# Kernel optimization log

Hardware: AMD Instinct MI355X
Metric: run time of the kernel (lower is better)

## Reference

```python
import jax, jax.numpy as jnp
import numpy as np

EPS = 1e-9

def setup_inputs() -> dict:
    key = jax.random.key(0)
    k1, k2 = jax.random.split(key)
    B = 1048576
    p1 = jax.random.uniform(k1, (B, 10), dtype=jnp.float32)
    p2 = jax.random.uniform(k2, (B, 10), dtype=jnp.float32)
    return {"p1": p1, "p2": p2}

def _sum_bin_matrix(dtype):
    # M[ij, k] = 1 if i + j == k, for flattened 10x10 outer product -> 19 bins
    sum_idx = (jnp.arange(10)[:, None] + jnp.arange(10)[None, :]).reshape(-1)  # [100]
    return (sum_idx[:, None] == jnp.arange(19)[None, :]).astype(dtype)  # [100,19]

def reference(p1, p2):
    B = p1.shape[0]
    # outer product of digit probabilities: T[b,i,j] = p1[b,i] * p2[b,j]
    T = (p1[:, :, None] * p2[:, None, :]).reshape(B, 100)  # [B,100]
    M = _sum_bin_matrix(p1.dtype)  # [100,19]
    probs = T @ M  # [B,19]: per-diagonal sums, P(sum=k)
    probs = probs / (probs.sum(axis=1, keepdims=True) + EPS)
    return probs
```

## Files before the change

kernel.cpp:

```cpp
#include <hip/hip_runtime.h>
#include <stddef.h>


#define EPS 1e-9f

constexpr int THREADS = 256;
constexpr int ROWS    = 256;

__global__ __launch_bounds__(THREADS)
void dpl_add_kernel(const float* __restrict__ p1,
                    const float* __restrict__ p2,
                    float* __restrict__ out,
                    int B) {
    __shared__ __align__(16) float sa[ROWS * 10];
    __shared__ __align__(16) float sb[ROWS * 10];
    __shared__ __align__(16) float so[ROWS * 19];

    const int tid  = threadIdx.x;
    const int row0 = blockIdx.x * ROWS;
    const bool full = (row0 + ROWS) <= B;

    if (full) {
        const float4* g1 = reinterpret_cast<const float4*>(p1 + (size_t)row0 * 10);
        const float4* g2 = reinterpret_cast<const float4*>(p2 + (size_t)row0 * 10);
        float4* s1 = reinterpret_cast<float4*>(sa);
        float4* s2 = reinterpret_cast<float4*>(sb);
        for (int i = tid; i < ROWS * 10 / 4; i += THREADS) {
            s1[i] = g1[i];
            s2[i] = g2[i];
        }
    } else {
        int n = B - row0; if (n < 0) n = 0;
        for (int i = tid; i < n * 10; i += THREADS) {
            sa[i] = p1[(size_t)row0 * 10 + i];
            sb[i] = p2[(size_t)row0 * 10 + i];
        }
    }
    __syncthreads();

    const int b = row0 + tid;
    float s[19];
    #pragma unroll
    for (int k = 0; k < 19; ++k) s[k] = 0.0f;

    if (b < B) {
        float a[10], c[10];
        #pragma unroll
        for (int i = 0; i < 10; ++i) {
            a[i] = sa[tid * 10 + i];
            c[i] = sb[tid * 10 + i];
        }
        #pragma unroll
        for (int i = 0; i < 10; ++i) {
            #pragma unroll
            for (int j = 0; j < 10; ++j) {
                s[i + j] = fmaf(a[i], c[j], s[i + j]);
            }
        }
        float tot = 0.0f;
        #pragma unroll
        for (int k = 0; k < 19; ++k) tot += s[k];
        const float den = tot + EPS;
        #pragma unroll
        for (int k = 0; k < 19; ++k) s[k] = s[k] / den;
    }

    #pragma unroll
    for (int k = 0; k < 19; ++k) so[tid * 19 + k] = s[k];
    __syncthreads();

    if (full) {
        float4* o4 = reinterpret_cast<float4*>(out + (size_t)row0 * 19);
        const float4* s4 = reinterpret_cast<const float4*>(so);
        for (int i = tid; i < ROWS * 19 / 4; i += THREADS) {
            o4[i] = s4[i];
        }
    } else {
        int n = B - row0; if (n < 0) n = 0;
        for (int i = tid; i < n * 19; i += THREADS) {
            out[(size_t)row0 * 19 + i] = so[i];
        }
    }
}

extern "C" void kernel_launch(void* const* d_in, const int* in_sizes, int n_in,
                              void* d_out, int out_size, void* d_ws, size_t ws_size,
                              hipStream_t stream) {
    const float* p1 = (const float*)d_in[0];
    const float* p2 = (const float*)d_in[1];
    float* out = (float*)d_out;
    const int B = in_sizes[0] / 10;

    const int grid = (B + ROWS - 1) / ROWS;
    dpl_add_kernel<<<grid, THREADS, 0, stream>>>(p1, p2, out, B);
}
```

Before: 146.0 us.

## Stage through per-wave LDS slices to remove block-wide barriers

Each wave now stages its own 64 rows through a private LDS slice, which is reused for both the inputs and the outputs, and synchronises with s_waitcnt plus sched_barrier instead of block-level __syncthreads. The smaller LDS footprint and the min-blocks launch bound are meant to raise occupancy and let waves proceed independently. The tail rows use a direct global-memory path. This relies on wave-local LDS ordering being sufficient without an explicit wave barrier, and input loads now use float2 instead of float4.

After: 145.3 us. About the same (-0.5%).

```diff
diff --git a/kernel.cpp b/kernel.cpp
--- a/kernel.cpp
+++ b/kernel.cpp
@@ -4,52 +4,51 @@
 
 #define EPS 1e-9f
 
-constexpr int THREADS = 256;
-constexpr int ROWS    = 256;
+constexpr int THREADS       = 256;
+constexpr int WAVES         = THREADS / 64;
+constexpr int ROWS          = THREADS;
+constexpr int ROWS_PER_WAVE = 64;
+constexpr int SLICE         = 1280;
 
-__global__ __launch_bounds__(THREADS)
+__global__ __launch_bounds__(THREADS, 8)
 void dpl_add_kernel(const float* __restrict__ p1,
                     const float* __restrict__ p2,
                     float* __restrict__ out,
                     int B) {
-    __shared__ __align__(16) float sa[ROWS * 10];
-    __shared__ __align__(16) float sb[ROWS * 10];
-    __shared__ __align__(16) float so[ROWS * 19];
+    __shared__ __align__(16) float lds[WAVES * SLICE];
 
-    const int tid  = threadIdx.x;
-    const int row0 = blockIdx.x * ROWS;
-    const bool full = (row0 + ROWS) <= B;
+    const int tid   = threadIdx.x;
+    const int lane  = tid & 63;
+    const int wid   = tid >> 6;
+    const int wrow0 = blockIdx.x * ROWS + wid * ROWS_PER_WAVE;
 
-    if (full) {
-        const float4* g1 = reinterpret_cast<const float4*>(p1 + (size_t)row0 * 10);
-        const float4* g2 = reinterpret_cast<const float4*>(p2 + (size_t)row0 * 10);
-        float4* s1 = reinterpret_cast<float4*>(sa);
-        float4* s2 = reinterpret_cast<float4*>(sb);
-        for (int i = tid; i < ROWS * 10 / 4; i += THREADS) {
-            s1[i] = g1[i];
-            s2[i] = g2[i];
+    float* slice = lds + wid * SLICE;
+
+    if (wrow0 + ROWS_PER_WAVE <= B) {
+        const float2* g1 = reinterpret_cast<const float2*>(p1 + (size_t)wrow0 * 10);
+        const float2* g2 = reinterpret_cast<const float2*>(p2 + (size_t)wrow0 * 10);
+        float2* s1 = reinterpret_cast<float2*>(slice);
+        float2* s2 = reinterpret_cast<float2*>(slice + 640);
+        #pragma unroll
+        for (int r = 0; r < 5; ++r) {
+            s1[r * 64 + lane] = g1[r * 64 + lane];
+            s2[r * 64 + lane] = g2[r * 64 + lane];
         }
-    } else {
-        int n = B - row0; if (n < 0) n = 0;
-        for (int i = tid; i < n * 10; i += THREADS) {
-            sa[i] = p1[(size_t)row0 * 10 + i];
-            sb[i] = p2[(size_t)row0 * 10 + i];
-        }
-    }
-    __syncthreads();
+        asm volatile("s_waitcnt lgkmcnt(0)" ::: "memory");
+        __builtin_amdgcn_sched_barrier(0);
 
-    const int b = row0 + tid;
-    float s[19];
-    #pragma unroll
-    for (int k = 0; k < 19; ++k) s[k] = 0.0f;
-
-    if (b < B) {
         float a[10], c[10];
         #pragma unroll
-        for (int i = 0; i < 10; ++i) {
-            a[i] = sa[tid * 10 + i];
-            c[i] = sb[tid * 10 + i];
+        for (int i = 0; i < 5; ++i) {
+            float2 va = reinterpret_cast<const float2*>(slice)[lane * 5 + i];
+            float2 vc = reinterpret_cast<const float2*>(slice + 640)[lane * 5 + i];
+            a[2 * i] = va.x; a[2 * i + 1] = va.y;
+            c[2 * i] = vc.x; c[2 * i + 1] = vc.y;
         }
+
+        float s[19];
+        #pragma unroll
+        for (int k = 0; k < 19; ++k) s[k] = 0.0f;
         #pragma unroll
         for (int i = 0; i < 10; ++i) {
             #pragma unroll
@@ -63,22 +62,40 @@
         const float den = tot + EPS;
         #pragma unroll
         for (int k = 0; k < 19; ++k) s[k] = s[k] / den;
-    }
 
-    #pragma unroll
-    for (int k = 0; k < 19; ++k) so[tid * 19 + k] = s[k];
-    __syncthreads();
+        asm volatile("s_waitcnt lgkmcnt(0)" ::: "memory");
+        __builtin_amdgcn_sched_barrier(0);
 
-    if (full) {
-        float4* o4 = reinterpret_cast<float4*>(out + (size_t)row0 * 19);
-        const float4* s4 = reinterpret_cast<const float4*>(so);
-        for (int i = tid; i < ROWS * 19 / 4; i += THREADS) {
-            o4[i] = s4[i];
+        #pragma unroll
+        for (int k = 0; k < 19; ++k) slice[lane * 19 + k] = s[k];
+
+        asm volatile("s_waitcnt lgkmcnt(0)" ::: "memory");
+        __builtin_amdgcn_sched_barrier(0);
+
+        float4* o4 = reinterpret_cast<float4*>(out + (size_t)wrow0 * 19);
+        const float4* s4 = reinterpret_cast<const float4*>(slice);
+        #pragma unroll
+        for (int r = 0; r < 5; ++r) {
+            int idx = r * 64 + lane;
+            if (idx < 304) o4[idx] = s4[idx];
         }
     } else {
-        int n = B - row0; if (n < 0) n = 0;
-        for (int i = tid; i < n * 19; i += THREADS) {
-            out[(size_t)row0 * 19 + i] = so[i];
+        const int b = wrow0 + lane;
+        if (b < B) {
+            float a[10], c[10];
+            for (int i = 0; i < 10; ++i) {
+                a[i] = p1[(size_t)b * 10 + i];
+                c[i] = p2[(size_t)b * 10 + i];
+            }
+            float s[19];
+            for (int k = 0; k < 19; ++k) s[k] = 0.0f;
+            for (int i = 0; i < 10; ++i)
+                for (int j = 0; j < 10; ++j)
+                    s[i + j] = fmaf(a[i], c[j], s[i + j]);
+            float tot = 0.0f;
+            for (int k = 0; k < 19; ++k) tot += s[k];
+            const float den = tot + EPS;
+            for (int k = 0; k < 19; ++k) out[(size_t)b * 19 + k] = s[k] / den;
         }
     }
 }
```

## Drop shared-memory staging and read/write rows directly per thread

Applied to the files above, without the earlier changes.

Removes the LDS staging of input rows and output rows. Each thread now loads its own 10-float rows with float2 loads and writes its 19 outputs with scalar stores straight to global memory, and both __syncthreads barriers are gone. This saves LDS traffic and synchronisation but replaces coalesced float4 global accesses with strided per-thread accesses (40-byte input stride, 76-byte output stride). That may waste memory transactions in a bandwidth-bound kernel.

Measured after the change: 157.4 us. 7.8% more time.

```diff
diff --git a/kernel.cpp b/kernel.cpp
--- a/kernel.cpp
+++ b/kernel.cpp
@@ -5,82 +5,45 @@
 #define EPS 1e-9f
 
 constexpr int THREADS = 256;
-constexpr int ROWS    = 256;
 
 __global__ __launch_bounds__(THREADS)
 void dpl_add_kernel(const float* __restrict__ p1,
                     const float* __restrict__ p2,
                     float* __restrict__ out,
                     int B) {
-    __shared__ __align__(16) float sa[ROWS * 10];
-    __shared__ __align__(16) float sb[ROWS * 10];
-    __shared__ __align__(16) float so[ROWS * 19];
+    const int b = blockIdx.x * THREADS + threadIdx.x;
+    if (b >= B) return;
 
-    const int tid  = threadIdx.x;
-    const int row0 = blockIdx.x * ROWS;
-    const bool full = (row0 + ROWS) <= B;
+    const float2* r1 = reinterpret_cast<const float2*>(p1 + (size_t)b * 10);
+    const float2* r2 = reinterpret_cast<const float2*>(p2 + (size_t)b * 10);
+    float a[10], c[10];
+    #pragma unroll
+    for (int i = 0; i < 5; ++i) {
+        float2 va = r1[i];
+        float2 vc = r2[i];
+        a[2 * i] = va.x; a[2 * i + 1] = va.y;
+        c[2 * i] = vc.x; c[2 * i + 1] = vc.y;
+    }
 
-    if (full) {
-        const float4* g1 = reinterpret_cast<const float4*>(p1 + (size_t)row0 * 10);
-        const float4* g2 = reinterpret_cast<const float4*>(p2 + (size_t)row0 * 10);
-        float4* s1 = reinterpret_cast<float4*>(sa);
-        float4* s2 = reinterpret_cast<float4*>(sb);
-        for (int i = tid; i < ROWS * 10 / 4; i += THREADS) {
-            s1[i] = g1[i];
-            s2[i] = g2[i];
-        }
-    } else {
-        int n = B - row0; if (n < 0) n = 0;
-        for (int i = tid; i < n * 10; i += THREADS) {
-            sa[i] = p1[(size_t)row0 * 10 + i];
-            sb[i] = p2[(size_t)row0 * 10 + i];
-        }
-    }
-    __syncthreads();
-
-    const int b = row0 + tid;
     float s[19];
     #pragma unroll
     for (int k = 0; k < 19; ++k) s[k] = 0.0f;
-
-    if (b < B) {
-        float a[10], c[10];
+    #pragma unroll
+    for (int i = 0; i < 10; ++i) {
         #pragma unroll
-        for (int i = 0; i < 10; ++i) {
-            a[i] = sa[tid * 10 + i];
-            c[i] = sb[tid * 10 + i];
+        for (int j = 0; j < 10; ++j) {
+            s[i + j] = fmaf(a[i], c[j], s[i + j]);
         }
-        #pragma unroll
-        for (int i = 0; i < 10; ++i) {
-            #pragma unroll
-            for (int j = 0; j < 10; ++j) {
-                s[i + j] = fmaf(a[i], c[j], s[i + j]);
-            }
-        }
-        float tot = 0.0f;
-        #pragma unroll
-        for (int k = 0; k < 19; ++k) tot += s[k];
-        const float den = tot + EPS;
-        #pragma unroll
-        for (int k = 0; k < 19; ++k) s[k] = s[k] / den;
     }
 
+    float tot = 0.0f;
     #pragma unroll
-    for (int k = 0; k < 19; ++k) so[tid * 19 + k] = s[k];
-    __syncthreads();
+    for (int k = 0; k < 19; ++k) tot += s[k];
+    const float den = tot + EPS;
 
-    if (full) {
-        float4* o4 = reinterpret_cast<float4*>(out + (size_t)row0 * 19);
-        const float4* s4 = reinterpret_cast<const float4*>(so);
-        for (int i = tid; i < ROWS * 19 / 4; i += THREADS) {
-            o4[i] = s4[i];
-        }
-    } else {
-        int n = B - row0; if (n < 0) n = 0;
-        for (int i = tid; i < n * 19; i += THREADS) {
-            out[(size_t)row0 * 19 + i] = so[i];
-        }
-    }
+    float* o = out + (size_t)b * 19;
+    #pragma unroll
+    for (int k = 0; k < 19; ++k) o[k] = s[k] / den;
 }
 
 extern "C" void kernel_launch(void* const* d_in, const int* in_sizes, int n_in,
@@ -91,6 +54,6 @@
     float* out = (float*)d_out;
     const int B = in_sizes[0] / 10;
 
-    const int grid = (B + ROWS - 1) / ROWS;
+    const int grid = (B + THREADS - 1) / THREADS;
     dpl_add_kernel<<<grid, THREADS, 0, stream>>>(p1, p2, out, B);
 }
```
